# Kernel tuning notes

Hardware: AMD Instinct MI355X
Metric: run time of the kernel (lower is better)

Reference implementation:

```python
import jax, jax.numpy as jnp
import numpy as np
from jax import lax

B, NPG = 128, 1024          # graphs, nodes per graph
N = B * NPG                  # total nodes
AVG_DEG = 8
E = N * AVG_DEG              # total edges
F_N, F_E = 128, 32           # node / edge feature dims
LATENT = [32, 32, 32, 1]
D = sum(LATENT)              # total_latent_dim = 97
K = 30                       # sort-pooling k
C1, C2, KW2 = 16, 32, 5      # conv1d channels / kernel
OUT = 2
DENSE = ((K - 2) // 2 + 1 - KW2 + 1) * C2  # 352


def setup_inputs() -> dict:
    key = jax.random.key(0)
    ks = jax.random.split(key, 12)
    inp = {}
    inp["node_feat"] = jax.random.normal(ks[0], (N, F_N), jnp.float32)
    inp["edge_feat"] = jax.random.normal(ks[1], (E, F_E), jnp.float32)
    inp["edge_index"] = jax.random.randint(ks[2], (2, E), 0, N)
    dims = [F_N + F_E] + LATENT
    for i in range(4):
        inp[f"W{i}"] = jax.random.normal(ks[3 + i], (dims[i], dims[i + 1]), jnp.float32) * 0.05
        inp[f"b{i}"] = jnp.zeros((dims[i + 1],), jnp.float32)
    inp["w_conv1"] = jax.random.normal(ks[7], (C1, 1, D), jnp.float32) * 0.05
    inp["b_conv1"] = jnp.zeros((C1,), jnp.float32)
    inp["w_conv2"] = jax.random.normal(ks[8], (C2, C1, KW2), jnp.float32) * 0.05
    inp["b_conv2"] = jnp.zeros((C2,), jnp.float32)
    inp["w_out"] = jax.random.normal(ks[9], (DENSE, OUT), jnp.float32) * 0.05
    inp["b_out"] = jnp.zeros((OUT,), jnp.float32)
    return inp


def _maxpool2(x):
    # MaxPool1d(2, 2) over last axis of [B, C, L]
    return lax.reduce_window(x, -jnp.inf, lax.max, (1, 1, 2), (1, 1, 2), "VALID")


def _forward(node_feat, edge_feat, W0, b0, W1, b1, W2, b2, W3, b3,
             w_conv1, b_conv1, w_conv2, b_conv2, w_out, b_out, edge_index):
    src, dst = edge_index[0], edge_index[1]
    # degree with self-loop, as in DGCNN (divide by deg after linear)
    deg = jnp.ones((N,), node_feat.dtype).at[dst].add(1.0)
    # e2npool: sum incident edge features onto destination nodes
    e2n = jax.ops.segment_sum(edge_feat, dst, num_segments=N)
    cur = jnp.concatenate([node_feat, e2n], axis=1)  # [N, F_N+F_E]
    hops = []
    for W, b in ((W0, b0), (W1, b1), (W2, b2), (W3, b3)):
        # (A + I) X  -> Linear -> / deg -> tanh
        pooled = jax.ops.segment_sum(cur[src], dst, num_segments=N) + cur
        cur = jnp.tanh((pooled @ W + b) / deg[:, None])
        hops.append(cur)
    feat = jnp.concatenate(hops, axis=1).reshape(B, NPG, D)  # [B, NPG, 97]
    # SortPooling: top-k nodes per graph by last latent channel
    _, idx = lax.top_k(feat[:, :, -1], K)                    # [B, K]
    sp = jnp.take_along_axis(feat, idx[:, :, None], axis=1)  # [B, K, D]
    x = sp.reshape(B, 1, K * D)
    x = lax.conv_general_dilated(x, w_conv1, (D,), "VALID",
                                 dimension_numbers=("NCH", "OIH", "NCH"))
    x = jax.nn.relu(x + b_conv1[None, :, None])  # [B, 16, 30]
    x = _maxpool2(x)                              # [B, 16, 15]
    x = lax.conv_general_dilated(x, w_conv2, (1,), "VALID",
                                 dimension_numbers=("NCH", "OIH", "NCH"))
    x = jax.nn.relu(x + b_conv2[None, :, None])  # [B, 32, 11]
    x = x.reshape(B, -1)                          # [B, 352]
    return jax.nn.relu(x @ w_out + b_out)         # [B, OUT]


def reference(node_feat, edge_feat, edge_index, W0, b0, W1, b1, W2, b2, W3, b3,
              w_conv1, b_conv1, w_conv2, b_conv2, w_out, b_out):
    return _forward(node_feat, edge_feat, W0, b0, W1, b1, W2, b2, W3, b3,
                    w_conv1, b_conv1, w_conv2, b_conv2, w_out, b_out, edge_index)
```

## Files before the change

### kernel.cpp

```cpp
#include <hip/hip_runtime.h>
#include <hip/hip_bf16.h>
#include <math.h>

#define N_NODES 131072
#define N_EDGES 1048576
#define B_GR    128
#define NPG_    1024
#define KTOP    30


__global__ __launch_bounds__(256) void k_zero(int* cnt) {
    int i = blockIdx.x * 256 + threadIdx.x;
    if (i < N_NODES) cnt[i] = 0;
}

__global__ __launch_bounds__(256) void k_count(const int* __restrict__ dst, int* __restrict__ cnt) {
    int e = blockIdx.x * 256 + threadIdx.x;
    if (e < N_EDGES) atomicAdd(&cnt[dst[e]], 1);
}

__global__ __launch_bounds__(256) void k_scan1(const int* __restrict__ cnt,
                                               int* __restrict__ row_start,
                                               int* __restrict__ blocksum) {
    __shared__ int s[256];
    int t = threadIdx.x;
    int i = blockIdx.x * 256 + t;
    int v = cnt[i];
    s[t] = v; __syncthreads();
    for (int o = 1; o < 256; o <<= 1) {
        int x = (t >= o) ? s[t - o] : 0;
        __syncthreads();
        s[t] += x;
        __syncthreads();
    }
    row_start[i] = s[t] - v;
    if (t == 255) blocksum[blockIdx.x] = s[t];
}

__global__ __launch_bounds__(512) void k_scan2(int* __restrict__ blocksum) {
    __shared__ int s[512];
    int t = threadIdx.x;
    int v = blocksum[t];
    s[t] = v; __syncthreads();
    for (int o = 1; o < 512; o <<= 1) {
        int x = (t >= o) ? s[t - o] : 0;
        __syncthreads();
        s[t] += x;
        __syncthreads();
    }
    blocksum[t] = s[t] - v;
}

__global__ __launch_bounds__(256) void k_scan3(int* __restrict__ row_start,
                                               const int* __restrict__ blocksum,
                                               int* __restrict__ cursor) {
    int i = blockIdx.x * 256 + threadIdx.x;
    int r = row_start[i] + blocksum[blockIdx.x];
    row_start[i] = r;
    cursor[i] = r;
}

__global__ __launch_bounds__(256) void k_fill(const int* __restrict__ src,
                                              const int* __restrict__ dst,
                                              int* __restrict__ cursor,
                                              int2* __restrict__ csr) {
    int e = blockIdx.x * 256 + threadIdx.x;
    if (e < N_EDGES) {
        int d = dst[e];
        int pos = atomicAdd(&cursor[d], 1);
        csr[pos] = make_int2(src[e], e);
    }
}


__global__ __launch_bounds__(256) void k_esum(const float* __restrict__ ef,
                                              const int* __restrict__ row_start,
                                              const int* __restrict__ cnt,
                                              const int2* __restrict__ csr,
                                              float* __restrict__ esum) {
    int g = threadIdx.x >> 5, j = threadIdx.x & 31;
    int n0 = (blockIdx.x * 8 + g) * 4;
    int st[4], ln[4];
    #pragma unroll
    for (int i = 0; i < 4; ++i) { st[i] = row_start[n0 + i]; ln[i] = cnt[n0 + i]; }
    float acc[4] = {0.f, 0.f, 0.f, 0.f};
    int base = 0;
    while ((ln[0] > base) | (ln[1] > base) | (ln[2] > base) | (ln[3] > base)) {
        int eid[4][8];
        #pragma unroll
        for (int i = 0; i < 4; ++i) {
            #pragma unroll
            for (int s = 0; s < 8; ++s) {
                int idx = base + s;
                int a = st[i] + ((idx < ln[i]) ? idx : 0);
                a = (a < N_EDGES) ? a : 0;
                eid[i][s] = csr[a].y;
            }
        }
        #pragma unroll
        for (int i = 0; i < 4; ++i) {
            #pragma unroll
            for (int s = 0; s < 8; ++s) {
                float v = ef[(size_t)eid[i][s] * 32 + j];
                acc[i] += ((base + s) < ln[i]) ? v : 0.f;
            }
        }
        base += 8;
    }
    #pragma unroll
    for (int i = 0; i < 4; ++i)
        esum[(size_t)(n0 + i) * 32 + j] = acc[i];
}


__global__ __launch_bounds__(256) void k_gemm160(const float* __restrict__ nf,
                                                 const float* __restrict__ esum,
                                                 const float* __restrict__ W0,
                                                 float* __restrict__ z0) {
    __shared__ float a[64 * 161];
    int tid = threadIdx.x;
    int n0 = blockIdx.x * 64;
    const float* nfb = nf + (size_t)n0 * 128;
    for (int f = tid; f < 8192; f += 256) {
        int n = f >> 7, k = f & 127;
        a[n * 161 + k] = nfb[f];
    }
    const float* esb = esum + (size_t)n0 * 32;
    for (int f = tid; f < 2048; f += 256) {
        int n = f >> 5, k = f & 31;
        a[n * 161 + 128 + k] = esb[f];
    }
    __syncthreads();
    int wv = __builtin_amdgcn_readfirstlane(tid >> 6);
    int lane = tid & 63;
    int c0 = wv * 8;
    float acc[8] = {0.f, 0.f, 0.f, 0.f, 0.f, 0.f, 0.f, 0.f};
    const float* ar = a + lane * 161;
    for (int k = 0; k < 160; ++k) {
        float av = ar[k];
        #pragma unroll
        for (int jj = 0; jj < 8; ++jj)
            acc[jj] += av * W0[k * 32 + c0 + jj];
    }
    float* zr = z0 + (size_t)(n0 + lane) * 32 + c0;
    *(float4*)zr = make_float4(acc[0], acc[1], acc[2], acc[3]);
    *(float4*)(zr + 4) = make_float4(acc[4], acc[5], acc[6], acc[7]);
}


__global__ __launch_bounds__(256) void k_layer(const float* __restrict__ zin,
                                               const int* __restrict__ row_start,
                                               const int* __restrict__ cnt,
                                               const int2* __restrict__ csr,
                                               const float* __restrict__ bias,
                                               const float* __restrict__ Wn,
                                               float* __restrict__ hout,
                                               float* __restrict__ znext) {
    __shared__ float Ws[1024];
    int tid = threadIdx.x;
    for (int f = tid; f < 1024; f += 256) Ws[f] = Wn[f];
    __syncthreads();
    int g = tid >> 5, j = tid & 31;
    int n0 = (blockIdx.x * 8 + g) * 4;
    int st[4], ln[4];
    #pragma unroll
    for (int i = 0; i < 4; ++i) { st[i] = row_start[n0 + i]; ln[i] = cnt[n0 + i]; }
    float acc[4];
    #pragma unroll
    for (int i = 0; i < 4; ++i) acc[i] = zin[(size_t)(n0 + i) * 32 + j];
    int base = 0;
    while ((ln[0] > base) | (ln[1] > base) | (ln[2] > base) | (ln[3] > base)) {
        int sid[4][8];
        #pragma unroll
        for (int i = 0; i < 4; ++i) {
            #pragma unroll
            for (int s = 0; s < 8; ++s) {
                int idx = base + s;
                int a = st[i] + ((idx < ln[i]) ? idx : 0);
                a = (a < N_EDGES) ? a : 0;
                sid[i][s] = csr[a].x;
            }
        }
        #pragma unroll
        for (int i = 0; i < 4; ++i) {
            #pragma unroll
            for (int s = 0; s < 8; ++s) {
                float v = zin[(size_t)sid[i][s] * 32 + j];
                acc[i] += ((base + s) < ln[i]) ? v : 0.f;
            }
        }
        base += 8;
    }
    float bj = bias[j];
    float h[4];
    #pragma unroll
    for (int i = 0; i < 4; ++i) {
        float deg = 1.f + (float)ln[i];
        h[i] = tanhf((acc[i] + bj) / deg);
        hout[(size_t)(n0 + i) * 32 + j] = h[i];
    }
    float z[4] = {0.f, 0.f, 0.f, 0.f};
    for (int k = 0; k < 32; ++k) {
        float w = Ws[k * 32 + j];
        #pragma unroll
        for (int i = 0; i < 4; ++i)
            z[i] += __shfl(h[i], k, 32) * w;
    }
    #pragma unroll
    for (int i = 0; i < 4; ++i)
        znext[(size_t)(n0 + i) * 32 + j] = z[i];
}


__global__ __launch_bounds__(256) void k_layer3(const float* __restrict__ zin,
                                                const int* __restrict__ row_start,
                                                const int* __restrict__ cnt,
                                                const int2* __restrict__ csr,
                                                const float* __restrict__ bias,
                                                const float* __restrict__ W3,
                                                float* __restrict__ hout,
                                                float* __restrict__ z3) {
    int g = threadIdx.x >> 5, j = threadIdx.x & 31;
    int n0 = (blockIdx.x * 8 + g) * 4;
    int st[4], ln[4];
    #pragma unroll
    for (int i = 0; i < 4; ++i) { st[i] = row_start[n0 + i]; ln[i] = cnt[n0 + i]; }
    float acc[4];
    #pragma unroll
    for (int i = 0; i < 4; ++i) acc[i] = zin[(size_t)(n0 + i) * 32 + j];
    int base = 0;
    while ((ln[0] > base) | (ln[1] > base) | (ln[2] > base) | (ln[3] > base)) {
        int sid[4][8];
        #pragma unroll
        for (int i = 0; i < 4; ++i) {
            #pragma unroll
            for (int s = 0; s < 8; ++s) {
                int idx = base + s;
                int a = st[i] + ((idx < ln[i]) ? idx : 0);
                a = (a < N_EDGES) ? a : 0;
                sid[i][s] = csr[a].x;
            }
        }
        #pragma unroll
        for (int i = 0; i < 4; ++i) {
            #pragma unroll
            for (int s = 0; s < 8; ++s) {
                float v = zin[(size_t)sid[i][s] * 32 + j];
                acc[i] += ((base + s) < ln[i]) ? v : 0.f;
            }
        }
        base += 8;
    }
    float bj = bias[j];
    float w3 = W3[j];
    #pragma unroll
    for (int i = 0; i < 4; ++i) {
        float deg = 1.f + (float)ln[i];
        float h = tanhf((acc[i] + bj) / deg);
        hout[(size_t)(n0 + i) * 32 + j] = h;
        float t = h * w3;
        #pragma unroll
        for (int o = 16; o; o >>= 1) t += __shfl_xor(t, o, 32);
        if (j == 0) z3[n0 + i] = t;
    }
}


__global__ __launch_bounds__(256) void k_g3(const float* __restrict__ z3,
                                            const int* __restrict__ row_start,
                                            const int* __restrict__ cnt,
                                            const int2* __restrict__ csr,
                                            const float* __restrict__ b3,
                                            float* __restrict__ val) {
    int n = blockIdx.x * 256 + threadIdx.x;
    int start = row_start[n], len = cnt[n];
    const int2* cs = csr + start;
    float s = z3[n];
    int i = 0;
    for (; i + 4 <= len; i += 4)
        s += z3[cs[i].x] + z3[cs[i + 1].x] + z3[cs[i + 2].x] + z3[cs[i + 3].x];
    for (; i < len; ++i) s += z3[cs[i].x];
    float deg = 1.f + (float)len;
    val[n] = tanhf((s + b3[0]) / deg);
}


__global__ __launch_bounds__(256) void k_head(const float* __restrict__ h0,
                                              const float* __restrict__ h1,
                                              const float* __restrict__ h2,
                                              const float* __restrict__ val,
                                              const float* __restrict__ wc1,
                                              const float* __restrict__ bc1,
                                              const float* __restrict__ wc2,
                                              const float* __restrict__ bc2,
                                              const float* __restrict__ wout,
                                              const float* __restrict__ bout,
                                              float* __restrict__ out) {
    __shared__ float vals[1024];
    __shared__ int selidx[KTOP];
    __shared__ float sp[KTOP * 97];
    __shared__ float y1[16 * 30];
    __shared__ float pool[16 * 15];
    __shared__ float y2[352];
    int b = blockIdx.x, tid = threadIdx.x;
    const float* vb = val + (size_t)b * NPG_;
    for (int u = tid; u < NPG_; u += 256) vals[u] = vb[u];
    __syncthreads();
    if (tid < 64) {
        unsigned long long keys[16];
        #pragma unroll
        for (int r = 0; r < 16; ++r) {
            int u = tid * 16 + r;
            unsigned int bb = __float_as_uint(vals[u]);
            unsigned int ord = (bb & 0x80000000u) ? ~bb : (bb | 0x80000000u);
            keys[r] = ((unsigned long long)ord << 32) |
                      (unsigned long long)(0xFFFFFFFFu - (unsigned int)u);
        }
        for (int k = 0; k < KTOP; ++k) {
            unsigned long long m = keys[0];
            #pragma unroll
            for (int r = 1; r < 16; ++r) m = (keys[r] > m) ? keys[r] : m;
            #pragma unroll
            for (int o = 32; o; o >>= 1) {
                unsigned long long t = __shfl_xor(m, o);
                m = (t > m) ? t : m;
            }
            int u = (int)(0xFFFFFFFFu - (unsigned int)(m & 0xFFFFFFFFull));
            if (tid == 0) selidx[k] = u;
            #pragma unroll
            for (int r = 0; r < 16; ++r)
                if (tid * 16 + r == u) keys[r] = 0ull;
        }
    }
    __syncthreads();
    size_t nb = (size_t)b * NPG_;
    for (int idx = tid; idx < KTOP * 32; idx += 256) {
        int t = idx >> 5, d = idx & 31;
        size_t s = (nb + (size_t)selidx[t]) * 32;
        sp[t * 97 + d]      = h0[s + d];
        sp[t * 97 + 32 + d] = h1[s + d];
        sp[t * 97 + 64 + d] = h2[s + d];
    }
    if (tid < KTOP) sp[tid * 97 + 96] = vb[selidx[tid]];
    __syncthreads();
    for (int idx = tid; idx < 480; idx += 256) {
        int t = idx >> 4, c = idx & 15;
        float acc = bc1[c];
        for (int d = 0; d < 97; ++d) acc += sp[t * 97 + d] * wc1[c * 97 + d];
        y1[c * 30 + t] = fmaxf(acc, 0.f);
    }
    __syncthreads();
    for (int idx = tid; idx < 240; idx += 256) {
        int c = idx / 15, u = idx - c * 15;
        pool[c * 15 + u] = fmaxf(y1[c * 30 + 2 * u], y1[c * 30 + 2 * u + 1]);
    }
    __syncthreads();
    for (int idx = tid; idx < 352; idx += 256) {
        int o = idx / 11, t = idx - o * 11;
        float acc = bc2[o];
        for (int i = 0; i < 16; ++i)
            for (int kk = 0; kk < 5; ++kk)
                acc += pool[i * 15 + t + kk] * wc2[(o * 16 + i) * 5 + kk];
        y2[idx] = fmaxf(acc, 0.f);
    }
    __syncthreads();
    if (tid < 2) {
        float acc = bout[tid];
        for (int m = 0; m < 352; ++m) acc += y2[m] * wout[m * 2 + tid];
        out[b * 2 + tid] = fmaxf(acc, 0.f);
    }
}


extern "C" void kernel_launch(void* const* d_in, const int* in_sizes, int n_in,
                              void* d_out, int out_size, void* d_ws, size_t ws_size,
                              hipStream_t stream) {
    const float* node_feat = (const float*)d_in[0];
    const float* edge_feat = (const float*)d_in[1];
    const int*   eidx      = (const int*)d_in[2];
    const float* W0 = (const float*)d_in[3];
    const float* b0 = (const float*)d_in[4];
    const float* W1 = (const float*)d_in[5];
    const float* b1 = (const float*)d_in[6];
    const float* W2 = (const float*)d_in[7];
    const float* b2 = (const float*)d_in[8];
    const float* W3 = (const float*)d_in[9];
    const float* b3 = (const float*)d_in[10];
    const float* wc1 = (const float*)d_in[11];
    const float* bc1 = (const float*)d_in[12];
    const float* wc2 = (const float*)d_in[13];
    const float* bc2 = (const float*)d_in[14];
    const float* wout = (const float*)d_in[15];
    const float* bout = (const float*)d_in[16];
    float* out = (float*)d_out;

    const int* src = eidx;
    const int* dst = eidx + N_EDGES;

    char* ws = (char*)d_ws;
    size_t off = 0;
    auto alloc = [&](size_t bytes) -> char* {
        char* p = ws + off;
        off += (bytes + 255) & ~(size_t)255;
        return p;
    };
    int* cnt       = (int*)alloc((size_t)N_NODES * 4);
    int* row_start = (int*)alloc((size_t)N_NODES * 4);
    int* cursor    = (int*)alloc((size_t)N_NODES * 4);
    int* blocksum  = (int*)alloc(512 * 4);
    int2* csr      = (int2*)alloc((size_t)N_EDGES * 8);
    float* esum    = (float*)alloc((size_t)N_NODES * 32 * 4);
    float* z0      = (float*)alloc((size_t)N_NODES * 32 * 4);
    float* z1      = (float*)alloc((size_t)N_NODES * 32 * 4);
    float* z2      = (float*)alloc((size_t)N_NODES * 32 * 4);
    float* h0      = (float*)alloc((size_t)N_NODES * 32 * 4);
    float* h1      = (float*)alloc((size_t)N_NODES * 32 * 4);
    float* h2      = (float*)alloc((size_t)N_NODES * 32 * 4);
    float* z3      = (float*)alloc((size_t)N_NODES * 4);
    float* val     = (float*)alloc((size_t)N_NODES * 4);
    (void)ws_size;

    k_zero<<<N_NODES / 256, 256, 0, stream>>>(cnt);
    k_count<<<N_EDGES / 256, 256, 0, stream>>>(dst, cnt);
    k_scan1<<<N_NODES / 256, 256, 0, stream>>>(cnt, row_start, blocksum);
    k_scan2<<<1, 512, 0, stream>>>(blocksum);
    k_scan3<<<N_NODES / 256, 256, 0, stream>>>(row_start, blocksum, cursor);
    k_fill<<<N_EDGES / 256, 256, 0, stream>>>(src, dst, cursor, csr);
    k_esum<<<N_NODES / 32, 256, 0, stream>>>(edge_feat, row_start, cnt, csr, esum);
    k_gemm160<<<N_NODES / 64, 256, 0, stream>>>(node_feat, esum, W0, z0);
    k_layer<<<N_NODES / 32, 256, 0, stream>>>(z0, row_start, cnt, csr, b0, W1, h0, z1);
    k_layer<<<N_NODES / 32, 256, 0, stream>>>(z1, row_start, cnt, csr, b1, W2, h1, z2);
    k_layer3<<<N_NODES / 32, 256, 0, stream>>>(z2, row_start, cnt, csr, b2, W3, h2, z3);
    k_g3<<<N_NODES / 256, 256, 0, stream>>>(z3, row_start, cnt, csr, b3, val);
    k_head<<<B_GR, 256, 0, stream>>>(h0, h1, h2, val, wc1, bc1, wc2, bc2, wout, bout, out);
}
```

Measured before the change: 598.5 us.

## Partition count/fill atomics by XCD and split CSR into separate src/eid arrays

k_count and k_fill now launch 2048 blocks. Each block scans 4096 edges and only performs atomics for destinations whose high bits (d>>14) match blockIdx&7. The intent is to keep each atomic target range on one XCD's L2 on MI355X, assuming round-robin block-to-XCD dispatch. The interleaved int2 CSR is split into separate csr_src and csr_eid arrays, so gather kernels load only the 4-byte field they need. The cost is that every dst value is now read eight times, and the XCD mapping assumption is not guaranteed.

```diff
diff --git a/kernel.cpp b/kernel.cpp
--- a/kernel.cpp
+++ b/kernel.cpp
@@ -15,8 +15,14 @@
 }
 
 __global__ __launch_bounds__(256) void k_count(const int* __restrict__ dst, int* __restrict__ cnt) {
-    int e = blockIdx.x * 256 + threadIdx.x;
-    if (e < N_EDGES) atomicAdd(&cnt[dst[e]], 1);
+    int xcd = blockIdx.x & 7;
+    int base = (blockIdx.x >> 3) * 4096 + threadIdx.x;
+    #pragma unroll
+    for (int it = 0; it < 16; ++it) {
+        int e = base + it * 256;
+        int d = __builtin_nontemporal_load(dst + e);
+        if ((d >> 14) == xcd) atomicAdd(&cnt[d], 1);
+    }
 }
 
 __global__ __launch_bounds__(256) void k_scan1(const int* __restrict__ cnt,
@@ -63,12 +69,20 @@
 __global__ __launch_bounds__(256) void k_fill(const int* __restrict__ src,
                                               const int* __restrict__ dst,
                                               int* __restrict__ cursor,
-                                              int2* __restrict__ csr) {
-    int e = blockIdx.x * 256 + threadIdx.x;
-    if (e < N_EDGES) {
-        int d = dst[e];
-        int pos = atomicAdd(&cursor[d], 1);
-        csr[pos] = make_int2(src[e], e);
+                                              int* __restrict__ csr_src,
+                                              int* __restrict__ csr_eid) {
+    int xcd = blockIdx.x & 7;
+    int base = (blockIdx.x >> 3) * 4096 + threadIdx.x;
+    #pragma unroll
+    for (int it = 0; it < 16; ++it) {
+        int e = base + it * 256;
+        int d = __builtin_nontemporal_load(dst + e);
+        if ((d >> 14) == xcd) {
+            int s = __builtin_nontemporal_load(src + e);
+            int pos = atomicAdd(&cursor[d], 1);
+            csr_src[pos] = s;
+            csr_eid[pos] = e;
+        }
     }
 }
 
@@ -76,7 +90,7 @@
 __global__ __launch_bounds__(256) void k_esum(const float* __restrict__ ef,
                                               const int* __restrict__ row_start,
                                               const int* __restrict__ cnt,
-                                              const int2* __restrict__ csr,
+                                              const int* __restrict__ csr_eid,
                                               float* __restrict__ esum) {
     int g = threadIdx.x >> 5, j = threadIdx.x & 31;
     int n0 = (blockIdx.x * 8 + g) * 4;
@@ -94,7 +108,7 @@
                 int idx = base + s;
                 int a = st[i] + ((idx < ln[i]) ? idx : 0);
                 a = (a < N_EDGES) ? a : 0;
-                eid[i][s] = csr[a].y;
+                eid[i][s] = csr_eid[a];
             }
         }
         #pragma unroll
@@ -151,7 +165,7 @@
 __global__ __launch_bounds__(256) void k_layer(const float* __restrict__ zin,
                                                const int* __restrict__ row_start,
                                                const int* __restrict__ cnt,
-                                               const int2* __restrict__ csr,
+                                               const int* __restrict__ csr_src,
                                                const float* __restrict__ bias,
                                                const float* __restrict__ Wn,
                                                float* __restrict__ hout,
@@ -178,7 +192,7 @@
                 int idx = base + s;
                 int a = st[i] + ((idx < ln[i]) ? idx : 0);
                 a = (a < N_EDGES) ? a : 0;
-                sid[i][s] = csr[a].x;
+                sid[i][s] = csr_src[a];
             }
         }
         #pragma unroll
@@ -215,7 +229,7 @@
 __global__ __launch_bounds__(256) void k_layer3(const float* __restrict__ zin,
                                                 const int* __restrict__ row_start,
                                                 const int* __restrict__ cnt,
-                                                const int2* __restrict__ csr,
+                                                const int* __restrict__ csr_src,
                                                 const float* __restrict__ bias,
                                                 const float* __restrict__ W3,
                                                 float* __restrict__ hout,
@@ -238,7 +252,7 @@
                 int idx = base + s;
                 int a = st[i] + ((idx < ln[i]) ? idx : 0);
                 a = (a < N_EDGES) ? a : 0;
-                sid[i][s] = csr[a].x;
+                sid[i][s] = csr_src[a];
             }
         }
         #pragma unroll
@@ -269,17 +283,17 @@
 __global__ __launch_bounds__(256) void k_g3(const float* __restrict__ z3,
                                             const int* __restrict__ row_start,
                                             const int* __restrict__ cnt,
-                                            const int2* __restrict__ csr,
+                                            const int* __restrict__ csr_src,
                                             const float* __restrict__ b3,
                                             float* __restrict__ val) {
     int n = blockIdx.x * 256 + threadIdx.x;
     int start = row_start[n], len = cnt[n];
-    const int2* cs = csr + start;
+    const int* cs = csr_src + start;
     float s = z3[n];
     int i = 0;
     for (; i + 4 <= len; i += 4)
-        s += z3[cs[i].x] + z3[cs[i + 1].x] + z3[cs[i + 2].x] + z3[cs[i + 3].x];
-    for (; i < len; ++i) s += z3[cs[i].x];
+        s += z3[cs[i]] + z3[cs[i + 1]] + z3[cs[i + 2]] + z3[cs[i + 3]];
+    for (; i < len; ++i) s += z3[cs[i]];
     float deg = 1.f + (float)len;
     val[n] = tanhf((s + b3[0]) / deg);
 }
@@ -408,7 +422,8 @@
     int* row_start = (int*)alloc((size_t)N_NODES * 4);
     int* cursor    = (int*)alloc((size_t)N_NODES * 4);
     int* blocksum  = (int*)alloc(512 * 4);
-    int2* csr      = (int2*)alloc((size_t)N_EDGES * 8);
+    int* csr_src   = (int*)alloc((size_t)N_EDGES * 4);
+    int* csr_eid   = (int*)alloc((size_t)N_EDGES * 4);
     float* esum    = (float*)alloc((size_t)N_NODES * 32 * 4);
     float* z0      = (float*)alloc((size_t)N_NODES * 32 * 4);
     float* z1      = (float*)alloc((size_t)N_NODES * 32 * 4);
@@ -421,16 +436,16 @@
     (void)ws_size;
 
     k_zero<<<N_NODES / 256, 256, 0, stream>>>(cnt);
-    k_count<<<N_EDGES / 256, 256, 0, stream>>>(dst, cnt);
+    k_count<<<2048, 256, 0, stream>>>(dst, cnt);
     k_scan1<<<N_NODES / 256, 256, 0, stream>>>(cnt, row_start, blocksum);
     k_scan2<<<1, 512, 0, stream>>>(blocksum);
     k_scan3<<<N_NODES / 256, 256, 0, stream>>>(row_start, blocksum, cursor);
-    k_fill<<<N_EDGES / 256, 256, 0, stream>>>(src, dst, cursor, csr);
-    k_esum<<<N_NODES / 32, 256, 0, stream>>>(edge_feat, row_start, cnt, csr, esum);
+    k_fill<<<2048, 256, 0, stream>>>(src, dst, cursor, csr_src, csr_eid);
+    k_esum<<<N_NODES / 32, 256, 0, stream>>>(edge_feat, row_start, cnt, csr_eid, esum);
     k_gemm160<<<N_NODES / 64, 256, 0, stream>>>(node_feat, esum, W0, z0);
-    k_layer<<<N_NODES / 32, 256, 0, stream>>>(z0, row_start, cnt, csr, b0, W1, h0, z1);
-    k_layer<<<N_NODES / 32, 256, 0, stream>>>(z1, row_start, cnt, csr, b1, W2, h1, z2);
-    k_layer3<<<N_NODES / 32, 256, 0, stream>>>(z2, row_start, cnt, csr, b2, W3, h2, z3);
-    k_g3<<<N_NODES / 256, 256, 0, stream>>>(z3, row_start, cnt, csr, b3, val);
+    k_layer<<<N_NODES / 32, 256, 0, stream>>>(z0, row_start, cnt, csr_src, b0, W1, h0, z1);
+    k_layer<<<N_NODES / 32, 256, 0, stream>>>(z1, row_start, cnt, csr_src, b1, W2, h1, z2);
+    k_layer3<<<N_NODES / 32, 256, 0, stream>>>(z2, row_start, cnt, csr_src, b2, W3, h2, z3);
+    k_g3<<<N_NODES / 256, 256, 0, stream>>>(z3, row_start, cnt, csr_src, b3, val);
     k_head<<<B_GR, 256, 0, stream>>>(h0, h1, h2, val, wc1, bc1, wc2, bc2, wout, bout, out);
 }
```

Measured after the change: 582.2 us. 2.7% less time.
